# Performance work log

Measured on AMD Instinct MI355X. Metric: run time of the kernel, lower is better.

## Reference

```python
import jax, jax.numpy as jnp
import numpy as np

T, B, L = 8192, 8, 1024
HID, H, KV, D = 2048, 16, 8, 128
G = H // KV
EPS = 1e-6
SCALE = 1.0 / float(np.sqrt(D))


def _rms(x, w):
    # RMSNorm over last dim (head_dim), eps=1e-6
    return x * jax.lax.rsqrt(jnp.mean(x * x, axis=-1, keepdims=True) + EPS) * w


def _rot_half(x):
    h = x.shape[-1] // 2
    return jnp.concatenate([-x[..., h:], x[..., :h]], axis=-1)


def setup_inputs() -> dict:
    key = jax.random.key(0)
    ks = jax.random.split(key, 12)
    inp = {}
    inp["packed_sequence"] = jax.random.normal(ks[0], (T, HID), jnp.float32)
    # rotary embeddings: per-sample positions 0..L-1, packed
    pos = jnp.tile(jnp.arange(L), B).astype(jnp.float32)
    inv = 1.0 / (10000.0 ** (jnp.arange(0, D, 2, dtype=jnp.float32) / D))
    fr = pos[:, None] * inv[None, :]
    emb = jnp.concatenate([fr, fr], axis=-1)  # [T, D]
    inp["cos"] = jnp.cos(emb)
    inp["sin"] = jnp.sin(emb)
    # per-sample causal float mask (additive): 0 allowed, -1e9 masked
    tril = jnp.tril(jnp.ones((L, L), bool))
    inp["attention_mask"] = jnp.broadcast_to(
        jnp.where(tril, 0.0, -1e9).astype(jnp.float32)[None], (B, L, L)
    )
    # disjoint und/gen routing indexes covering all T tokens
    inp["und_idx"] = jnp.arange(0, T, 2, dtype=jnp.int32)
    inp["gen_idx"] = jnp.arange(1, T, 2, dtype=jnp.int32)
    s = 0.02

    def lin(k, o, i):
        return jax.random.normal(k, (o, i), jnp.float32) * s

    kk = jax.random.split(ks[1], 8)
    inp["Wq_u"] = lin(kk[0], H * D, HID); inp["bq_u"] = jnp.zeros((H * D,), jnp.float32)
    inp["Wk_u"] = lin(kk[1], KV * D, HID); inp["bk_u"] = jnp.zeros((KV * D,), jnp.float32)
    inp["Wv_u"] = lin(kk[2], KV * D, HID); inp["bv_u"] = jnp.zeros((KV * D,), jnp.float32)
    inp["Wo_u"] = lin(kk[3], HID, H * D)
    inp["Wq_g"] = lin(kk[4], H * D, HID); inp["bq_g"] = jnp.zeros((H * D,), jnp.float32)
    inp["Wk_g"] = lin(kk[5], KV * D, HID); inp["bk_g"] = jnp.zeros((KV * D,), jnp.float32)
    inp["Wv_g"] = lin(kk[6], KV * D, HID); inp["bv_g"] = jnp.zeros((KV * D,), jnp.float32)
    inp["Wo_g"] = lin(kk[7], HID, H * D)
    inp["qn_u"] = jnp.ones((D,), jnp.float32); inp["kn_u"] = jnp.ones((D,), jnp.float32)
    inp["qn_g"] = jnp.ones((D,), jnp.float32); inp["kn_g"] = jnp.ones((D,), jnp.float32)
    return inp


def reference(packed_sequence, cos, sin, attention_mask, und_idx, gen_idx,
              Wq_u, bq_u, Wk_u, bk_u, Wv_u, bv_u, Wo_u,
              Wq_g, bq_g, Wk_g, bk_g, Wv_g, bv_g, Wo_g,
              qn_u, kn_u, qn_g, kn_g):
    x_u = packed_sequence[und_idx]  # [T/2, HID]
    x_g = packed_sequence[gen_idx]

    def route(Wu, bu, Wg, bg, width):
        out = jnp.zeros((T, width), packed_sequence.dtype)
        out = out.at[und_idx].set(x_u @ Wu.T + bu)
        out = out.at[gen_idx].set(x_g @ Wg.T + bg)
        return out

    q = route(Wq_u, bq_u, Wq_g, bq_g, H * D).reshape(T, H, D)
    k = route(Wk_u, bk_u, Wk_g, bk_g, KV * D).reshape(T, KV, D)
    v = route(Wv_u, bv_u, Wv_g, bv_g, KV * D).reshape(T, KV, D)

    # routed per-head QK RMSNorm (separate und/gen weights)
    qn = jnp.zeros_like(q).at[und_idx].set(_rms(q[und_idx], qn_u)).at[gen_idx].set(_rms(q[gen_idx], qn_g))
    kn = jnp.zeros_like(k).at[und_idx].set(_rms(k[und_idx], kn_u)).at[gen_idx].set(_rms(k[gen_idx], kn_g))

    c, s = cos[:, None, :], sin[:, None, :]  # unsqueeze_dim=1
    q = qn * c + _rot_half(qn) * s
    k = kn * c + _rot_half(kn) * s

    # GQA expansion: kv head i -> heads i*G..i*G+G-1
    k = jnp.repeat(k, G, axis=1)  # [T, H, D]
    v = jnp.repeat(v, G, axis=1)

    qb = q.reshape(B, L, H, D)
    kb = k.reshape(B, L, H, D)
    vb = v.reshape(B, L, H, D)

    scores = jnp.einsum('blhd,bmhd->bhlm', qb, kb) * SCALE
    scores = scores + attention_mask[:, None, :, :]
    p = jax.nn.softmax(scores, axis=-1)
    o = jnp.einsum('bhlm,bmhd->blhd', p, vb).reshape(T, H * D)

    out = jnp.zeros((T, HID), packed_sequence.dtype)
    out = out.at[und_idx].set(o[und_idx] @ Wo_u.T)
    out = out.at[gen_idx].set(o[gen_idx] @ Wo_g.T)
    return out
```

## Files before the change

### kernel.cpp

```cpp
#include <hip/hip_runtime.h>
#include <hip/hip_bf16.h>
#include <stdint.h>
#include <math.h>

#define T_TOK 8192
#define HID   2048
#define NH    16
#define NKV   8
#define HD    128
#define LSEQ  1024
#define BATCH 8
#define QKV_N 4096
#define KDIM  2048
#define SCALE 0.08838834764831845f

typedef __hip_bfloat16 bf16;
typedef __bf16 bf16x8 __attribute__((ext_vector_type(8)));
typedef float  f32x4  __attribute__((ext_vector_type(4)));

typedef const void __attribute__((address_space(1)))* gas_ptr;
typedef void       __attribute__((address_space(3)))* las_ptr;

__device__ __forceinline__ float b2f(bf16 x) { return __bfloat162float(x); }
__device__ __forceinline__ bf16  f2b(float x) { return __float2bfloat16(x); }
__device__ __forceinline__ unsigned short f2u(float x) {
    union { bf16 b; unsigned short u; } c; c.b = __float2bfloat16(x); return c.u;
}

__device__ __forceinline__ bf16x8 ld16(const bf16* p) {
    union { uint4 u; bf16x8 v; } c;
    c.u = *reinterpret_cast<const uint4*>(p);
    return c.v;
}

__device__ __forceinline__ void cp16(void* lds, const void* g) {
    __builtin_amdgcn_global_load_lds((gas_ptr)g, (las_ptr)lds, 16, 0, 0);
}

__global__ __launch_bounds__(256) void k_f2b(const float* __restrict__ in,
                                             bf16* __restrict__ out, int n) {
    int i = blockIdx.x * blockDim.x + threadIdx.x;
    int stride = gridDim.x * blockDim.x;
    const float4* in4 = (const float4*)in;
    ushort4* out4 = (ushort4*)out;
    int n4 = n >> 2;
    for (int j = i; j < n4; j += stride) {
        float4 v = in4[j];
        ushort4 o;
        o.x = f2u(v.x); o.y = f2u(v.y); o.z = f2u(v.z); o.w = f2u(v.w);
        out4[j] = o;
    }
}

__global__ __launch_bounds__(256) void k_mod(const int* __restrict__ und,
                                             const int* __restrict__ gen,
                                             int* __restrict__ mod, int n) {
    int i = blockIdx.x * blockDim.x + threadIdx.x;
    if (i < n) { mod[und[i]] = 0; mod[gen[i]] = 1; }
}

template<int EPI>
__global__ __launch_bounds__(256)
void k_gemm(const bf16* __restrict__ A,
            const bf16* __restrict__ Bw_u, const bf16* __restrict__ Bw_g,
            const int* __restrict__ und, const int* __restrict__ gen,
            const float* __restrict__ bq_u, const float* __restrict__ bk_u,
            const float* __restrict__ bv_u,
            const float* __restrict__ bq_g, const float* __restrict__ bk_g,
            const float* __restrict__ bv_g,
            bf16* __restrict__ outB, float* __restrict__ outF, int ntilesN) {
    __shared__ bf16 sA[128][32];
    __shared__ bf16 sB[128][32];

    int modg = blockIdx.y;
    const bf16* Bw = modg ? Bw_g : Bw_u;
    const int* idx = modg ? gen : und;
    const float* bq = modg ? bq_g : bq_u;
    const float* bk = modg ? bk_g : bk_u;
    const float* bv = modg ? bv_g : bv_u;

    int tile = blockIdx.x;
    int tn = tile % ntilesN, tm = tile / ntilesN;
    int tid = threadIdx.x;
    int w = tid >> 6, lane = tid & 63;
    int l16 = lane & 15, l4 = lane >> 4;
    int wrow = w >> 1, wcol = w & 1;

    const bf16* pA[2]; const bf16* pB[2];
    uint32_t ldsOff[2];
#pragma unroll
    for (int it = 0; it < 2; ++it) {
        int c = it * 256 + w * 64 + lane;
        int row = c >> 2, kc = (c & 3) * 8;
        pA[it] = A + (size_t)idx[tm * 128 + row] * KDIM + kc;
        pB[it] = Bw + (size_t)(tn * 128 + row) * KDIM + kc;
        ldsOff[it] = (uint32_t)(it * 256 + w * 64) * 16;
    }
    char* sAb = (char*)&sA[0][0];
    char* sBb = (char*)&sB[0][0];

    f32x4 zero = {0.f, 0.f, 0.f, 0.f};
    f32x4 acc[4][4];
#pragma unroll
    for (int m = 0; m < 4; ++m)
#pragma unroll
        for (int n = 0; n < 4; ++n) acc[m][n] = zero;

    for (int k0 = 0; k0 < KDIM; k0 += 32) {
        cp16(sAb + ldsOff[0], pA[0] + k0);
        cp16(sAb + ldsOff[1], pA[1] + k0);
        cp16(sBb + ldsOff[0], pB[0] + k0);
        cp16(sBb + ldsOff[1], pB[1] + k0);
        __syncthreads();
        bf16x8 af[4], bfr[4];
#pragma unroll
        for (int m = 0; m < 4; ++m) af[m] = ld16(&sA[wrow * 64 + m * 16 + l16][l4 * 8]);
#pragma unroll
        for (int n = 0; n < 4; ++n) bfr[n] = ld16(&sB[wcol * 64 + n * 16 + l16][l4 * 8]);
#pragma unroll
        for (int m = 0; m < 4; ++m)
#pragma unroll
            for (int n = 0; n < 4; ++n)
                acc[m][n] = __builtin_amdgcn_mfma_f32_16x16x32_bf16(af[m], bfr[n], acc[m][n], 0, 0, 0);
        __syncthreads();
    }

    int rowbase = tm * 128 + wrow * 64;
    int colbase = tn * 128 + wcol * 64;
#pragma unroll
    for (int m = 0; m < 4; ++m) {
#pragma unroll
        for (int r = 0; r < 4; ++r) {
            int row = rowbase + m * 16 + l4 * 4 + r;
            int token = idx[row];
#pragma unroll
            for (int n = 0; n < 4; ++n) {
                int col = colbase + n * 16 + l16;
                float v = acc[m][n][r];
                if (EPI == 0) {
                    float bias = (col < 2048) ? bq[col]
                               : (col < 3072) ? bk[col - 2048] : bv[col - 3072];
                    outB[(size_t)token * QKV_N + col] = f2b(v + bias);
                } else {
                    outF[(size_t)token * HID + col] = v;
                }
            }
        }
    }
}

__global__ __launch_bounds__(256)
void k_normrope(const bf16* __restrict__ qkv,
                const float* __restrict__ cosT, const float* __restrict__ sinT,
                const int* __restrict__ mod,
                const float* __restrict__ qn_u, const float* __restrict__ qn_g,
                const float* __restrict__ kn_u, const float* __restrict__ kn_g,
                bf16* __restrict__ Qo, bf16* __restrict__ Ko) {
    int t = blockIdx.x;
    int tid = threadIdx.x;
    int w = tid >> 6, lane = tid & 63;
    int m = mod[t];
    int b = t >> 10, pos = t & 1023;
    const bf16* row = qkv + (size_t)t * QKV_N;
    int d0 = 2 * lane, d1 = 2 * lane + 1;
    float c0 = cosT[(size_t)t * HD + d0], c1 = cosT[(size_t)t * HD + d1];
    float s0 = sinT[(size_t)t * HD + d0], s1 = sinT[(size_t)t * HD + d1];
    float sgn = (lane < 32) ? -1.f : 1.f;
    const float* qw = m ? qn_g : qn_u;
    const float* kw = m ? kn_g : kn_u;

    for (int u = w; u < 24; u += 4) {
        float v0 = b2f(row[u * HD + d0]);
        float v1 = b2f(row[u * HD + d1]);
        float ss = v0 * v0 + v1 * v1;
#pragma unroll
        for (int msk = 1; msk < 64; msk <<= 1) ss += __shfl_xor(ss, msk);
        float rs = rsqrtf(ss * (1.0f / HD) + 1e-6f);
        const float* wsc = (u < 16) ? qw : kw;
        float n0 = v0 * rs * wsc[d0], n1 = v1 * rs * wsc[d1];
        float o0 = __shfl_xor(n0, 32), o1 = __shfl_xor(n1, 32);
        float r0 = n0 * c0 + sgn * o0 * s0;
        float r1 = n1 * c1 + sgn * o1 * s1;
        if (u < 16) {
            size_t o = ((size_t)(b * NH + u) * LSEQ + pos) * HD;
            Qo[o + d0] = f2b(r0); Qo[o + d1] = f2b(r1);
        } else {
            size_t o = ((size_t)(b * NKV + (u - 16)) * LSEQ + pos) * HD;
            Ko[o + d0] = f2b(r0); Ko[o + d1] = f2b(r1);
        }
    }
}

__global__ __launch_bounds__(256)
void k_vt(const bf16* __restrict__ qkv, bf16* __restrict__ Vt) {
    __shared__ bf16 lds[64][72];
    int bk = blockIdx.x;
    int b = bk >> 3, kv = bk & 7;
    int pos0 = blockIdx.y * 64;
    int d0 = blockIdx.z * 64;
    int tid = threadIdx.x;

#pragma unroll
    for (int it = 0; it < 2; ++it) {
        int c = tid + it * 256;
        int row = c >> 3, col8 = (c & 7) * 8;
        const bf16* src = qkv + (size_t)(b * LSEQ + pos0 + row) * QKV_N
                        + 3072 + kv * HD + d0 + col8;
        *reinterpret_cast<uint4*>(&lds[row][col8]) = *reinterpret_cast<const uint4*>(src);
    }
    __syncthreads();

#pragma unroll
    for (int it = 0; it < 2; ++it) {
        int c = tid + it * 256;
        int drow = c & 63, pos8 = (c >> 6) * 8;
        union { unsigned short s[8]; uint4 u; } g;
#pragma unroll
        for (int j = 0; j < 8; ++j)
            g.s[j] = *reinterpret_cast<const unsigned short*>(&lds[pos8 + j][drow]);
        bf16* dst = Vt + ((size_t)bk * HD + d0 + drow) * LSEQ + pos0 + pos8;
        *reinterpret_cast<uint4*>(dst) = g.u;
    }
}

__global__ __launch_bounds__(256)
void k_attn(const bf16* __restrict__ Q, const bf16* __restrict__ K,
            const bf16* __restrict__ Vt, bf16* __restrict__ O) {
    int bid = blockIdx.x;
    int p = bid & 3;
    int h = (bid >> 2) & 15;
    int b = bid >> 6;
    int tid = threadIdx.x;
    int w = tid >> 6, lane = tid & 63;
    int l16 = lane & 15, l4 = lane >> 4;
    int j = p * 4 + w;

    const bf16* qhb = Q + (size_t)(b * NH + h) * LSEQ * HD;
    int kv = h >> 1;
    const bf16* kb = K + (size_t)(b * NKV + kv) * LSEQ * HD;
    const bf16* vtb = Vt + (size_t)(b * NKV + kv) * HD * LSEQ;

    __shared__ bf16 Pl[4][32][72];

    f32x4 zero = {0.f, 0.f, 0.f, 0.f};

#pragma unroll 1
    for (int half = 0; half < 2; ++half) {
        int rowblk = half ? (31 - j) : j;
        int q0 = rowblk * 32;
        int kend = q0 + 32;

        bf16x8 qf[2][4];
#pragma unroll
        for (int rf = 0; rf < 2; ++rf)
#pragma unroll
            for (int c = 0; c < 4; ++c)
                qf[rf][c] = ld16(qhb + (size_t)(q0 + rf * 16 + l16) * HD + c * 32 + l4 * 8);

        f32x4 oacc[2][8];
#pragma unroll
        for (int rf = 0; rf < 2; ++rf)
#pragma unroll
            for (int d = 0; d < 8; ++d) oacc[rf][d] = zero;
        float mr[2][4], lr[2][4];
#pragma unroll
        for (int rf = 0; rf < 2; ++rf)
#pragma unroll
            for (int r = 0; r < 4; ++r) { mr[rf][r] = -INFINITY; lr[rf][r] = 0.f; }

        for (int kt = 0; kt < kend; kt += 64) {
            f32x4 s[2][4];
#pragma unroll
            for (int rf = 0; rf < 2; ++rf)
#pragma unroll
                for (int kf = 0; kf < 4; ++kf) s[rf][kf] = zero;
#pragma unroll
            for (int c = 0; c < 4; ++c) {
                bf16x8 kf4[4];
#pragma unroll
                for (int kf = 0; kf < 4; ++kf)
                    kf4[kf] = ld16(kb + (size_t)(kt + kf * 16 + l16) * HD + c * 32 + l4 * 8);
#pragma unroll
                for (int rf = 0; rf < 2; ++rf)
#pragma unroll
                    for (int kf = 0; kf < 4; ++kf)
                        s[rf][kf] = __builtin_amdgcn_mfma_f32_16x16x32_bf16(qf[rf][c], kf4[kf], s[rf][kf], 0, 0, 0);
            }
#pragma unroll
            for (int rf = 0; rf < 2; ++rf) {
#pragma unroll
                for (int r = 0; r < 4; ++r) {
                    int qrow = q0 + rf * 16 + l4 * 4 + r;
                    float sc[4];
                    float rm = -1e30f;
#pragma unroll
                    for (int kf = 0; kf < 4; ++kf) {
                        int key = kt + kf * 16 + l16;
                        sc[kf] = (key <= qrow) ? s[rf][kf][r] * SCALE : -1e30f;
                        rm = fmaxf(rm, sc[kf]);
                    }
#pragma unroll
                    for (int msk = 1; msk < 16; msk <<= 1) rm = fmaxf(rm, __shfl_xor(rm, msk));
                    float mn = fmaxf(mr[rf][r], rm);
                    float corr = __expf(mr[rf][r] - mn);
                    mr[rf][r] = mn;
                    float rsum = 0.f;
#pragma unroll
                    for (int kf = 0; kf < 4; ++kf) {
                        float pv = __expf(sc[kf] - mn);
                        rsum += pv;
                        Pl[w][rf * 16 + l4 * 4 + r][kf * 16 + l16] = f2b(pv);
                    }
#pragma unroll
                    for (int msk = 1; msk < 16; msk <<= 1) rsum += __shfl_xor(rsum, msk);
                    lr[rf][r] = lr[rf][r] * corr + rsum;
#pragma unroll
                    for (int d = 0; d < 8; ++d) oacc[rf][d][r] *= corr;
                }
            }
            bf16x8 pf[2][2];
#pragma unroll
            for (int rf = 0; rf < 2; ++rf)
#pragma unroll
                for (int ks = 0; ks < 2; ++ks)
                    pf[rf][ks] = ld16(&Pl[w][rf * 16 + l16][ks * 32 + l4 * 8]);
#pragma unroll
            for (int dt = 0; dt < 8; ++dt) {
#pragma unroll
                for (int ks = 0; ks < 2; ++ks) {
                    bf16x8 vfr = ld16(vtb + (size_t)(dt * 16 + l16) * LSEQ + kt + ks * 32 + l4 * 8);
#pragma unroll
                    for (int rf = 0; rf < 2; ++rf)
                        oacc[rf][dt] = __builtin_amdgcn_mfma_f32_16x16x32_bf16(pf[rf][ks], vfr, oacc[rf][dt], 0, 0, 0);
                }
            }
        }

#pragma unroll
        for (int rf = 0; rf < 2; ++rf)
#pragma unroll
            for (int r = 0; r < 4; ++r) lr[rf][r] = 1.0f / lr[rf][r];
        int trow = b * LSEQ + q0;
#pragma unroll
        for (int rf = 0; rf < 2; ++rf)
#pragma unroll
            for (int dt = 0; dt < 8; ++dt)
#pragma unroll
                for (int r = 0; r < 4; ++r) {
                    int t = trow + rf * 16 + l4 * 4 + r;
                    O[(size_t)t * HID + h * HD + dt * 16 + l16] = f2b(oacc[rf][dt][r] * lr[rf][r]);
                }
    }
}

extern "C" void kernel_launch(void* const* d_in, const int* in_sizes, int n_in,
                              void* d_out, int out_size, void* d_ws, size_t ws_size,
                              hipStream_t stream) {
    const float* x    = (const float*)d_in[0];
    const float* cosT = (const float*)d_in[1];
    const float* sinT = (const float*)d_in[2];
    const int* und = (const int*)d_in[4];
    const int* gen = (const int*)d_in[5];
    const float* Wq_u = (const float*)d_in[6];
    const float* bq_u = (const float*)d_in[7];
    const float* Wk_u = (const float*)d_in[8];
    const float* bk_u = (const float*)d_in[9];
    const float* Wv_u = (const float*)d_in[10];
    const float* bv_u = (const float*)d_in[11];
    const float* Wo_u = (const float*)d_in[12];
    const float* Wq_g = (const float*)d_in[13];
    const float* bq_g = (const float*)d_in[14];
    const float* Wk_g = (const float*)d_in[15];
    const float* bk_g = (const float*)d_in[16];
    const float* Wv_g = (const float*)d_in[17];
    const float* bv_g = (const float*)d_in[18];
    const float* Wo_g = (const float*)d_in[19];
    const float* qn_u = (const float*)d_in[20];
    const float* kn_u = (const float*)d_in[21];
    const float* qn_g = (const float*)d_in[22];
    const float* kn_g = (const float*)d_in[23];
    float* out = (float*)d_out;

    char* ws = (char*)d_ws;
    size_t off = 0;
    auto alloc = [&](size_t bytes) -> void* {
        void* p = ws + off;
        off += (bytes + 255) & ~(size_t)255;
        return p;
    };
    bf16* xb      = (bf16*)alloc((size_t)T_TOK * HID * 2);
    bf16* Wqkv_u  = (bf16*)alloc((size_t)QKV_N * KDIM * 2);
    bf16* Wqkv_g  = (bf16*)alloc((size_t)QKV_N * KDIM * 2);
    bf16* Wob_u   = (bf16*)alloc((size_t)HID * HID * 2);
    bf16* Wob_g   = (bf16*)alloc((size_t)HID * HID * 2);
    int*  mod     = (int*)alloc((size_t)T_TOK * 4);
    bf16* qkv     = (bf16*)alloc((size_t)T_TOK * QKV_N * 2);
    bf16* Qa      = (bf16*)alloc((size_t)BATCH * NH  * LSEQ * HD * 2);
    bf16* Ka      = (bf16*)alloc((size_t)BATCH * NKV * LSEQ * HD * 2);
    bf16* Vt      = (bf16*)alloc((size_t)BATCH * NKV * HD * LSEQ * 2);
    bf16* Ob      = (bf16*)alloc((size_t)T_TOK * HID * 2);
    (void)ws_size; (void)in_sizes; (void)n_in; (void)out_size;

    k_f2b<<<1024, 256, 0, stream>>>(x, xb, T_TOK * HID);
    k_f2b<<<1024, 256, 0, stream>>>(Wq_u, Wqkv_u,               2048 * 2048);
    k_f2b<<<1024, 256, 0, stream>>>(Wk_u, Wqkv_u + 2048 * 2048, 1024 * 2048);
    k_f2b<<<1024, 256, 0, stream>>>(Wv_u, Wqkv_u + 3072 * 2048, 1024 * 2048);
    k_f2b<<<1024, 256, 0, stream>>>(Wq_g, Wqkv_g,               2048 * 2048);
    k_f2b<<<1024, 256, 0, stream>>>(Wk_g, Wqkv_g + 2048 * 2048, 1024 * 2048);
    k_f2b<<<1024, 256, 0, stream>>>(Wv_g, Wqkv_g + 3072 * 2048, 1024 * 2048);
    k_f2b<<<1024, 256, 0, stream>>>(Wo_u, Wob_u, 2048 * 2048);
    k_f2b<<<1024, 256, 0, stream>>>(Wo_g, Wob_g, 2048 * 2048);
    k_mod<<<16, 256, 0, stream>>>(und, gen, mod, T_TOK / 2);

    k_gemm<0><<<dim3(32 * 32, 2), 256, 0, stream>>>(
        xb, Wqkv_u, Wqkv_g, und, gen, bq_u, bk_u, bv_u, bq_g, bk_g, bv_g,
        qkv, nullptr, 32);

    k_normrope<<<T_TOK, 256, 0, stream>>>(qkv, cosT, sinT, mod,
                                          qn_u, qn_g, kn_u, kn_g, Qa, Ka);
    k_vt<<<dim3(BATCH * NKV, LSEQ / 64, HD / 64), 256, 0, stream>>>(qkv, Vt);

    k_attn<<<BATCH * NH * 4, 256, 0, stream>>>(Qa, Ka, Vt, Ob);

    k_gemm<1><<<dim3(32 * 16, 2), 256, 0, stream>>>(
        Ob, Wob_u, Wob_g, und, gen, nullptr, nullptr, nullptr,
        nullptr, nullptr, nullptr, nullptr, out, 16);
}
```

Baseline: 546.6 us.

## Rewrite routed GEMM with 256x256 tiles, double-buffered LDS and swizzle

Replaces the 128x128 GEMM, which issued one synchronous K=32 step per iteration, with a 512-thread 256x256-tile kernel. It stages K=64 slices into double-buffered 128KB dynamic LDS with an XOR swizzle to avoid bank conflicts, and prefetches two stages ahead using vmcnt waits. It also remaps block IDs for L2 locality and raises wave priority around the MFMA bursts. The aim is more reuse per loaded byte and memory latency hidden behind compute, at the cost of fewer blocks (lower occupancy) and heavy LDS and register use.

```diff
diff --git a/kernel.cpp b/kernel.cpp
--- a/kernel.cpp
+++ b/kernel.cpp
@@ -12,6 +12,7 @@
 #define BATCH 8
 #define QKV_N 4096
 #define KDIM  2048
+#define NTK   32
 #define SCALE 0.08838834764831845f
 
 typedef __hip_bfloat16 bf16;
@@ -60,17 +61,16 @@
 }
 
 template<int EPI>
-__global__ __launch_bounds__(256)
-void k_gemm(const bf16* __restrict__ A,
-            const bf16* __restrict__ Bw_u, const bf16* __restrict__ Bw_g,
-            const int* __restrict__ und, const int* __restrict__ gen,
-            const float* __restrict__ bq_u, const float* __restrict__ bk_u,
-            const float* __restrict__ bv_u,
-            const float* __restrict__ bq_g, const float* __restrict__ bk_g,
-            const float* __restrict__ bv_g,
-            bf16* __restrict__ outB, float* __restrict__ outF, int ntilesN) {
-    __shared__ bf16 sA[128][32];
-    __shared__ bf16 sB[128][32];
+__global__ __launch_bounds__(512)
+void k_gemm256(const bf16* __restrict__ A,
+               const bf16* __restrict__ Bw_u, const bf16* __restrict__ Bw_g,
+               const int* __restrict__ und, const int* __restrict__ gen,
+               const float* __restrict__ bq_u, const float* __restrict__ bk_u,
+               const float* __restrict__ bv_u,
+               const float* __restrict__ bq_g, const float* __restrict__ bk_g,
+               const float* __restrict__ bv_g,
+               bf16* __restrict__ outB, float* __restrict__ outF) {
+    extern __shared__ char smem[];
 
     int modg = blockIdx.y;
     const bf16* Bw = modg ? Bw_g : Bw_u;
@@ -79,56 +79,89 @@
     const float* bk = modg ? bk_g : bk_u;
     const float* bv = modg ? bv_g : bv_u;
 
-    int tile = blockIdx.x;
-    int tn = tile % ntilesN, tm = tile / ntilesN;
+    int gx = gridDim.x;
+    int bid = blockIdx.x;
+    int sw = (bid & 7) * (gx >> 3) + (bid >> 3);
+    int tn = sw >> 4;
+    int tm = sw & 15;
+
     int tid = threadIdx.x;
     int w = tid >> 6, lane = tid & 63;
     int l16 = lane & 15, l4 = lane >> 4;
-    int wrow = w >> 1, wcol = w & 1;
-
-    const bf16* pA[2]; const bf16* pB[2];
-    uint32_t ldsOff[2];
-#pragma unroll
-    for (int it = 0; it < 2; ++it) {
-        int c = it * 256 + w * 64 + lane;
-        int row = c >> 2, kc = (c & 3) * 8;
-        pA[it] = A + (size_t)idx[tm * 128 + row] * KDIM + kc;
-        pB[it] = Bw + (size_t)(tn * 128 + row) * KDIM + kc;
-        ldsOff[it] = (uint32_t)(it * 256 + w * 64) * 16;
-    }
-    char* sAb = (char*)&sA[0][0];
-    char* sBb = (char*)&sB[0][0];
-
-    f32x4 zero = {0.f, 0.f, 0.f, 0.f};
-    f32x4 acc[4][4];
-#pragma unroll
-    for (int m = 0; m < 4; ++m)
-#pragma unroll
-        for (int n = 0; n < 4; ++n) acc[m][n] = zero;
-
-    for (int k0 = 0; k0 < KDIM; k0 += 32) {
-        cp16(sAb + ldsOff[0], pA[0] + k0);
-        cp16(sAb + ldsOff[1], pA[1] + k0);
-        cp16(sBb + ldsOff[0], pB[0] + k0);
-        cp16(sBb + ldsOff[1], pB[1] + k0);
-        __syncthreads();
-        bf16x8 af[4], bfr[4];
-#pragma unroll
-        for (int m = 0; m < 4; ++m) af[m] = ld16(&sA[wrow * 64 + m * 16 + l16][l4 * 8]);
-#pragma unroll
-        for (int n = 0; n < 4; ++n) bfr[n] = ld16(&sB[wcol * 64 + n * 16 + l16][l4 * 8]);
-#pragma unroll
-        for (int m = 0; m < 4; ++m)
+    int wm = w >> 2, wn = w & 3;
+
+    int srow = tid >> 3;
+    int schunk = (tid & 7) ^ (srow & 7);
+    const bf16* aSrc[4];
+    const bf16* bSrc[4];
+#pragma unroll
+    for (int i = 0; i < 4; ++i) {
+        int ar = tm * 256 + i * 64 + srow;
+        aSrc[i] = A + (size_t)idx[ar] * KDIM + schunk * 8;
+        bSrc[i] = Bw + (size_t)(tn * 256 + i * 64 + srow) * KDIM + schunk * 8;
+    }
+
+    auto STAGE = [&](int t) {
+        char* Ab = smem + (t & 1) * 65536;
+        char* Bb = Ab + 32768;
+#pragma unroll
+        for (int i = 0; i < 4; ++i) {
+            cp16(Ab + i * 8192 + w * 1024, aSrc[i] + t * 64);
+            cp16(Bb + i * 8192 + w * 1024, bSrc[i] + t * 64);
+        }
+    };
+
+    f32x4 acc[8][4];
+#pragma unroll
+    for (int m = 0; m < 8; ++m)
+#pragma unroll
+        for (int n = 0; n < 4; ++n) acc[m][n] = {0.f, 0.f, 0.f, 0.f};
+
+    STAGE(0);
+    STAGE(1);
+
+    uint32_t aRowByte = (uint32_t)(wm * 128 + l16) * 128;
+    uint32_t bRowByte = (uint32_t)(wn * 64 + l16) * 128;
+    uint32_t rx = (uint32_t)(l16 & 7);
+
+#pragma unroll 1
+    for (int t = 0; t < NTK; ++t) {
+        if (t < NTK - 1) asm volatile("s_waitcnt vmcnt(8)" ::: "memory");
+        else             asm volatile("s_waitcnt vmcnt(0)" ::: "memory");
+        __builtin_amdgcn_s_barrier();
+        asm volatile("" ::: "memory");
+
+        const char* Ab = smem + (t & 1) * 65536;
+        const char* Bb = Ab + 32768;
+#pragma unroll
+        for (int kk = 0; kk < 2; ++kk) {
+            uint32_t cByte = ((((uint32_t)(kk << 2) | l4) ^ rx) << 4);
+            bf16x8 af[8], bfr[4];
+#pragma unroll
+            for (int m = 0; m < 8; ++m)
+                af[m] = ld16((const bf16*)(Ab + aRowByte + m * 2048 + cByte));
 #pragma unroll
             for (int n = 0; n < 4; ++n)
-                acc[m][n] = __builtin_amdgcn_mfma_f32_16x16x32_bf16(af[m], bfr[n], acc[m][n], 0, 0, 0);
-        __syncthreads();
-    }
-
-    int rowbase = tm * 128 + wrow * 64;
-    int colbase = tn * 128 + wcol * 64;
-#pragma unroll
-    for (int m = 0; m < 4; ++m) {
+                bfr[n] = ld16((const bf16*)(Bb + bRowByte + n * 2048 + cByte));
+            __builtin_amdgcn_s_setprio(1);
+#pragma unroll
+            for (int m = 0; m < 8; ++m)
+#pragma unroll
+                for (int n = 0; n < 4; ++n)
+                    acc[m][n] = __builtin_amdgcn_mfma_f32_16x16x32_bf16(af[m], bfr[n], acc[m][n], 0, 0, 0);
+            __builtin_amdgcn_s_setprio(0);
+        }
+
+        asm volatile("" ::: "memory");
+        __builtin_amdgcn_s_barrier();
+        asm volatile("" ::: "memory");
+        if (t + 2 < NTK) STAGE(t + 2);
+    }
+
+    int rowbase = tm * 256 + wm * 128;
+    int colbase = tn * 256 + wn * 64;
+#pragma unroll
+    for (int m = 0; m < 8; ++m) {
 #pragma unroll
         for (int r = 0; r < 4; ++r) {
             int row = rowbase + m * 16 + l4 * 4 + r;
@@ -401,6 +434,11 @@
     bf16* Ob      = (bf16*)alloc((size_t)T_TOK * HID * 2);
     (void)ws_size; (void)in_sizes; (void)n_in; (void)out_size;
 
+    (void)hipFuncSetAttribute((const void*)k_gemm256<0>,
+                              hipFuncAttributeMaxDynamicSharedMemorySize, 131072);
+    (void)hipFuncSetAttribute((const void*)k_gemm256<1>,
+                              hipFuncAttributeMaxDynamicSharedMemorySize, 131072);
+
     k_f2b<<<1024, 256, 0, stream>>>(x, xb, T_TOK * HID);
     k_f2b<<<1024, 256, 0, stream>>>(Wq_u, Wqkv_u,               2048 * 2048);
     k_f2b<<<1024, 256, 0, stream>>>(Wk_u, Wqkv_u + 2048 * 2048, 1024 * 2048);
@@ -412,9 +450,9 @@
     k_f2b<<<1024, 256, 0, stream>>>(Wo_g, Wob_g, 2048 * 2048);
     k_mod<<<16, 256, 0, stream>>>(und, gen, mod, T_TOK / 2);
 
-    k_gemm<0><<<dim3(32 * 32, 2), 256, 0, stream>>>(
+    k_gemm256<0><<<dim3(16 * 16, 2), 512, 131072, stream>>>(
         xb, Wqkv_u, Wqkv_g, und, gen, bq_u, bk_u, bv_u, bq_g, bk_g, bv_g,
-        qkv, nullptr, 32);
+        qkv, nullptr);
 
     k_normrope<<<T_TOK, 256, 0, stream>>>(qkv, cosT, sinT, mod,
                                           qn_u, qn_g, kn_u, kn_g, Qa, Ka);
@@ -422,7 +460,7 @@
 
     k_attn<<<BATCH * NH * 4, 256, 0, stream>>>(Qa, Ka, Vt, Ob);
 
-    k_gemm<1><<<dim3(32 * 16, 2), 256, 0, stream>>>(
+    k_gemm256<1><<<dim3(8 * 16, 2), 512, 131072, stream>>>(
         Ob, Wob_u, Wob_g, und, gen, nullptr, nullptr, nullptr,
-        nullptr, nullptr, nullptr, nullptr, out, 16);
-}
+        nullptr, nullptr, nullptr, nullptr, out);
+}
```

After: 493.3 us. 9.7% less time.
